# Kernel tuning notes

Hardware: AMD Instinct MI355X
Metric: run time of the kernel (lower is better)

## Reference

```python
import jax, jax.numpy as jnp
import numpy as np

N_NODES = 100000
D_IN = 128
H_DIM = 128
N_EDGES = 1600000


def _gcn_conv(x, src, dst, dinv, W, b):
    # PyG GCNConv(improved=True): h = x @ W; out = A_hat h + b,
    # A_hat = D^{-1/2} (A + 2I) D^{-1/2}
    h = x @ W                                   # [N, H]
    norm = dinv[src] * dinv[dst]                # [E]
    agg = jnp.zeros_like(h).at[dst].add(h[src] * norm[:, None])
    agg = agg + h * (2.0 * dinv * dinv)[:, None]  # self-loop, weight 2.0
    return agg + b


def setup_inputs() -> dict:
    key = jax.random.key(0)
    ks = jax.random.split(key, 12)
    s = 1.0 / np.sqrt(D_IN)
    sh = 1.0 / np.sqrt(2 * H_DIM)
    inp = {
        "x": jax.random.normal(ks[0], (N_NODES, D_IN), jnp.float32),
        "edge_index": jax.random.randint(ks[1], (2, N_EDGES), 0, N_NODES, jnp.int64),
        # GCNConv weights (in -> hidden), bias
        "Wz": jax.random.uniform(ks[2], (D_IN, H_DIM), jnp.float32, -s, s),
        "bz": jnp.zeros((H_DIM,), jnp.float32),
        "Wr": jax.random.uniform(ks[3], (D_IN, H_DIM), jnp.float32, -s, s),
        "br": jnp.zeros((H_DIM,), jnp.float32),
        "Wh": jax.random.uniform(ks[4], (D_IN, H_DIM), jnp.float32, -s, s),
        "bh": jnp.zeros((H_DIM,), jnp.float32),
        # TGCN gate linears: Linear(2h, h)
        "lzW": jax.random.uniform(ks[5], (2 * H_DIM, H_DIM), jnp.float32, -sh, sh),
        "lzb": jax.random.uniform(ks[6], (H_DIM,), jnp.float32, -sh, sh),
        "lrW": jax.random.uniform(ks[7], (2 * H_DIM, H_DIM), jnp.float32, -sh, sh),
        "lrb": jax.random.uniform(ks[8], (H_DIM,), jnp.float32, -sh, sh),
        "lhW": jax.random.uniform(ks[9], (2 * H_DIM, H_DIM), jnp.float32, -sh, sh),
        "lhb": jax.random.uniform(ks[10], (H_DIM,), jnp.float32, -sh, sh),
        # final linear2: hidden -> 1
        "W2": jax.random.uniform(ks[11], (H_DIM, 1), jnp.float32, -1 / np.sqrt(H_DIM), 1 / np.sqrt(H_DIM)),
        "b2": jnp.zeros((1,), jnp.float32),
    }
    return inp


def reference(x, edge_index, Wz, bz, Wr, br, Wh, bh, lzW, lzb, lrW, lrb, lhW, lhb, W2, b2):
    src, dst = edge_index[0], edge_index[1]
    n = x.shape[0]
    # improved GCN norm: deg includes self-loop weight 2
    deg = jnp.zeros((n,), x.dtype).at[dst].add(jnp.ones_like(src, x.dtype)) + 2.0
    dinv = jnp.where(deg > 0, deg ** -0.5, 0.0)
    # TGCN cell with H0 = 0
    H0 = jnp.zeros((n, Wz.shape[1]), x.dtype)
    Z = jax.nn.sigmoid(jnp.concatenate([_gcn_conv(x, src, dst, dinv, Wz, bz), H0], axis=1) @ lzW + lzb)
    R = jax.nn.sigmoid(jnp.concatenate([_gcn_conv(x, src, dst, dinv, Wr, br), H0], axis=1) @ lrW + lrb)
    Ht = jnp.tanh(jnp.concatenate([_gcn_conv(x, src, dst, dinv, Wh, bh), H0 * R], axis=1) @ lhW + lhb)
    H = Z * H0 + (1.0 - Z) * Ht
    # forward: relu output is discarded (y = h overwrites), then linear2
    return H @ W2 + b2
```

## Files before the change

kernel.cpp:

```cpp
#include <hip/hip_runtime.h>
#include <math.h>

#define D 128
#define BSHIFT 9
#define NB 196
#define EPT 7
#define P1B 241
#define CAPB 80
#define PSTRIDE (P1B * CAPB)
#define ECAP 9216
#define P2B NB
#define XCB2 3125
#define PRB 32

typedef __attribute__((ext_vector_type(8))) short s8v;
typedef __attribute__((ext_vector_type(8))) unsigned short us8;
typedef __attribute__((ext_vector_type(4))) unsigned short us4;
typedef __attribute__((ext_vector_type(4))) float f4v;

__device__ __forceinline__ float bf2f(unsigned short u) {
    union { unsigned int i; float f; } v; v.i = ((unsigned int)u) << 16; return v.f;
}
__device__ __forceinline__ unsigned short f2bf(float f) {
    union { float f; unsigned int i; } v; v.f = f;
    unsigned int r = v.i + 0x7FFFu + ((v.i >> 16) & 1u);
    return (unsigned short)(r >> 16);
}

__global__ __launch_bounds__(1024) void k_part1(
    const int* __restrict__ src, const int* __restrict__ dst, int E,
    unsigned int* __restrict__ pairs, int* __restrict__ runlen) {
    __shared__ int cnt[256];
    __shared__ int loff[256];
    __shared__ unsigned int stage[EPT * 1024];
    int bx = blockIdx.x, tid = threadIdx.x;

    unsigned int pk[EPT]; int rkbk[EPT];
    int e0 = bx * (EPT * 1024) + tid;
    if (tid < 256) cnt[tid] = 0;
    __syncthreads();
    #pragma unroll
    for (int i = 0; i < EPT; ++i) {
        int e = e0 + i * 1024;
        bool ok = e < E;
        int d = ok ? dst[e] : 0;
        int s = ok ? src[e] : 0;
        int bk = d >> BSHIFT;
        pk[i] = ((unsigned int)(d & ((1 << BSHIFT) - 1)) << 17) | (unsigned int)s;
        int r = ok ? atomicAdd(&cnt[bk], 1) : 0;
        rkbk[i] = ok ? ((bk << 16) | r) : -1;
    }
    __syncthreads();
    if (tid < 64) {
        int v0 = cnt[tid * 4], v1 = cnt[tid * 4 + 1], v2 = cnt[tid * 4 + 2], v3 = cnt[tid * 4 + 3];
        int s = v0 + v1 + v2 + v3;
        int sc = s;
        #pragma unroll
        for (int off = 1; off < 64; off <<= 1) {
            int o = __shfl_up(sc, off, 64);
            if (tid >= off) sc += o;
        }
        int excl = sc - s;
        loff[tid * 4]     = excl;
        loff[tid * 4 + 1] = excl + v0;
        loff[tid * 4 + 2] = excl + v0 + v1;
        loff[tid * 4 + 3] = excl + v0 + v1 + v2;
    }
    __syncthreads();
    #pragma unroll
    for (int i = 0; i < EPT; ++i) {
        if (rkbk[i] >= 0) {
            int bk = rkbk[i] >> 16;
            stage[loff[bk] + (rkbk[i] & 0xffff)] = pk[i];
        }
    }
    if (tid < 256) runlen[bx * 256 + tid] = cnt[tid];
    __syncthreads();
    int wv = tid >> 6, lane = tid & 63;
    for (int b = wv; b < 256; b += 16) {
        int len = cnt[b];
        if (len == 0) continue;
        int lo = loff[b];
        unsigned int gbase = (unsigned int)b * PSTRIDE + (unsigned int)bx * CAPB;
        for (int j = lane; j < len; j += 64)
            pairs[gbase + j] = stage[lo + j];
    }
}

__global__ __launch_bounds__(1024) void k_mid(
    const unsigned int* __restrict__ pairs, const int* __restrict__ runlen,
    int N,
    int* __restrict__ rowptr, int* __restrict__ deg, float* __restrict__ dinv,
    int* __restrict__ esrc,
    const float* __restrict__ x, unsigned short* __restrict__ xb, int n4,
    const float* __restrict__ Wz, const float* __restrict__ bz,
    const float* __restrict__ lzW, const float* __restrict__ lzb,
    const float* __restrict__ Wh, const float* __restrict__ bh,
    const float* __restrict__ lhW, const float* __restrict__ lhb,
    unsigned short* __restrict__ Mt, float* __restrict__ c) {
    __shared__ int cnt2[512];
    __shared__ int lcur[512];
    __shared__ int rl[256];
    __shared__ int sstage[ECAP];
    __shared__ int stot;
    int bx = blockIdx.x, tid = threadIdx.x;

    if (bx < P2B) {
        int b = bx;
        int n0 = b << BSHIFT;
        int nn = min(N - n0, 1 << BSHIFT);
        long pb = (long)b * PSTRIDE;
        int wv = tid >> 6, lane = tid & 63;

        if (tid < 256) rl[tid] = (tid < P1B) ? runlen[tid * 256 + b] : 0;
        if (tid < 512) cnt2[tid] = 0;
        __syncthreads();
        for (int r = wv; r < P1B; r += 16) {
            int len = rl[r];
            long rb = pb + r * CAPB;
            for (int j = lane; j < len; j += 64)
                atomicAdd(&cnt2[pairs[rb + j] >> 17], 1);
        }
        __syncthreads();
        if (tid < 64) {
            int v[8]; int s = 0;
            #pragma unroll
            for (int k = 0; k < 8; ++k) { v[k] = cnt2[tid * 8 + k]; s += v[k]; }
            int sc = s;
            #pragma unroll
            for (int off = 1; off < 64; off <<= 1) {
                int o = __shfl_up(sc, off, 64);
                if (tid >= off) sc += o;
            }
            int excl = sc - s;
            if (tid == 63) stot = sc;
            #pragma unroll
            for (int k = 0; k < 8; ++k) {
                int node = tid * 8 + k;
                lcur[node] = excl;
                if (node < nn) {
                    rowptr[n0 + node] = b * ECAP + excl;
                    deg[n0 + node]    = v[k];
                    dinv[n0 + node]   = rsqrtf((float)v[k] + 2.0f);
                }
                excl += v[k];
            }
        }
        __syncthreads();
        for (int r = wv; r < P1B; r += 16) {
            int len = rl[r];
            long rb = pb + r * CAPB;
            for (int j = lane; j < len; j += 64) {
                unsigned int p = pairs[rb + j];
                int pos = atomicAdd(&lcur[p >> 17], 1);
                sstage[pos] = (int)(p & 0x1FFFFu);
            }
        }
        __syncthreads();
        int tot = stot;
        for (int i = tid; i < tot; i += 1024)
            esrc[b * ECAP + i] = sstage[i];
    } else if (bx < P2B + XCB2) {
        int i = (bx - P2B) * 1024 + tid;
        if (i < n4) {
            float4 v = ((const float4*)x)[i];
            us4 o;
            o[0] = f2bf(v.x); o[1] = f2bf(v.y); o[2] = f2bf(v.z); o[3] = f2bf(v.w);
            ((us4*)xb)[i] = o;
        }
    } else {
        int k = (bx - (P2B + XCB2)) * 4 + (tid >> 8);
        int j = tid & 255;
        int jj = j & 127;
        const float* W = (j < 128) ? Wz : Wh;
        const float* L = (j < 128) ? lzW : lhW;
        float s = 0.f;
        for (int t = 0; t < 128; ++t) s += W[k * 128 + t] * L[t * 128 + jj];
        Mt[(size_t)j * 128 + k] = f2bf(s);
        if (k == 0) {
            const float* b  = (j < 128) ? bz  : bh;
            const float* lb = (j < 128) ? lzb : lhb;
            float cs = lb[jj];
            for (int t = 0; t < 128; ++t) cs += b[t] * L[t * 128 + jj];
            c[j] = cs;
        }
    }
}

__global__ __launch_bounds__(256) void k_gather(const unsigned short* __restrict__ xb,
                                                const int* __restrict__ esrc,
                                                const int* __restrict__ rowptr,
                                                const int* __restrict__ deg,
                                                const float* __restrict__ dinv,
                                                unsigned short* __restrict__ xab, int N) {
    int node = (blockIdx.x * blockDim.x + threadIdx.x) >> 5;
    int sub  = threadIdx.x & 31;
    if (node >= N) return;
    int eo = sub >> 4, cs = sub & 15;
    int start = rowptr[node];
    int end = start + deg[node];
    float dd = dinv[node];
    us8 xs = {0, 0, 0, 0, 0, 0, 0, 0};
    if (eo == 0) xs = *(const us8*)(xb + (size_t)node * D + cs * 8);
    float acc[8];
    #pragma unroll
    for (int j = 0; j < 8; ++j) acc[j] = 0.f;

    for (int base = start; base < end; base += 32) {
        int cnt = min(32, end - base);
        int myedge = 0; float mynorm = 0.f;
        if (sub < cnt) { myedge = esrc[base + sub]; mynorm = dinv[myedge]; }
        int npairs = (cnt + 1) >> 1;
        int i = 0;
        for (; i + 7 < npairs; i += 8) {
            int i0 = 2 * i + eo;
            int se[8]; float we[8];
            #pragma unroll
            for (int u = 0; u < 8; ++u) {
                se[u] = __shfl(myedge, i0 + 2 * u, 32);
                we[u] = __shfl(mynorm, i0 + 2 * u, 32);
            }
            us8 v[8];
            #pragma unroll
            for (int u = 0; u < 8; ++u)
                v[u] = *(const us8*)(xb + (size_t)se[u] * D + cs * 8);
            #pragma unroll
            for (int u = 0; u < 8; ++u) {
                #pragma unroll
                for (int j = 0; j < 8; ++j) acc[j] += bf2f(v[u][j]) * we[u];
            }
        }
        for (; i + 3 < npairs; i += 4) {
            int i0 = 2 * i + eo;
            int   s0 = __shfl(myedge, i0,     32); float w0 = __shfl(mynorm, i0,     32);
            int   s1 = __shfl(myedge, i0 + 2, 32); float w1 = __shfl(mynorm, i0 + 2, 32);
            int   s2 = __shfl(myedge, i0 + 4, 32); float w2 = __shfl(mynorm, i0 + 4, 32);
            int   s3 = __shfl(myedge, i0 + 6, 32); float w3 = __shfl(mynorm, i0 + 6, 32);
            us8 v0 = *(const us8*)(xb + (size_t)s0 * D + cs * 8);
            us8 v1 = *(const us8*)(xb + (size_t)s1 * D + cs * 8);
            us8 v2 = *(const us8*)(xb + (size_t)s2 * D + cs * 8);
            us8 v3 = *(const us8*)(xb + (size_t)s3 * D + cs * 8);
            #pragma unroll
            for (int j = 0; j < 8; ++j) acc[j] += bf2f(v0[j]) * w0;
            #pragma unroll
            for (int j = 0; j < 8; ++j) acc[j] += bf2f(v1[j]) * w1;
            #pragma unroll
            for (int j = 0; j < 8; ++j) acc[j] += bf2f(v2[j]) * w2;
            #pragma unroll
            for (int j = 0; j < 8; ++j) acc[j] += bf2f(v3[j]) * w3;
        }
        for (; i < npairs; ++i) {
            int i0 = 2 * i + eo;
            int   s0 = __shfl(myedge, i0, 32); float w0 = __shfl(mynorm, i0, 32);
            us8 v0 = *(const us8*)(xb + (size_t)s0 * D + cs * 8);
            #pragma unroll
            for (int j = 0; j < 8; ++j) acc[j] += bf2f(v0[j]) * w0;
        }
    }
    #pragma unroll
    for (int j = 0; j < 8; ++j) acc[j] += __shfl_xor(acc[j], 16);
    if (eo == 0) {
        float sfac = 2.f * dd * dd;
        us8 r;
        #pragma unroll
        for (int j = 0; j < 8; ++j) r[j] = f2bf(acc[j] * dd + bf2f(xs[j]) * sfac);
        *(us8*)(xab + (size_t)node * D + cs * 8) = r;
    }
}

#define ASTRIDE 136
__global__ __launch_bounds__(256, 4) void k_ep_mfma(
    const unsigned short* __restrict__ xab, const unsigned short* __restrict__ Mt,
    const float* __restrict__ c, const float* __restrict__ W2,
    const float* __restrict__ b2, float* __restrict__ out, int N) {
    __shared__ unsigned short Ast[64 * ASTRIDE];
    __shared__ float pbuf[4][64];

    int tid = threadIdx.x;
    int n0 = blockIdx.x * 64;
    int wv = tid >> 6;
    int lane = tid & 63;
    int l = lane & 15, q = lane >> 4;

    #pragma unroll
    for (int j = 0; j < 4; ++j) {
        int idx = tid + 256 * j;
        int row = idx >> 4, c16 = idx & 15;
        us8 v = {0, 0, 0, 0, 0, 0, 0, 0};
        if (n0 + row < N) v = *(const us8*)(xab + (size_t)(n0 + row) * D + c16 * 8);
        *(us8*)&Ast[row * ASTRIDE + c16 * 8] = v;
    }
    __syncthreads();

    int tz0 = 2 * wv;
    f4v acc[4][4];
    #pragma unroll
    for (int i = 0; i < 4; ++i)
        #pragma unroll
        for (int nt = 0; nt < 4; ++nt) acc[i][nt] = (f4v){0.f, 0.f, 0.f, 0.f};

    const unsigned short* Bb = Mt + (size_t)l * 128 + q * 8;

    #pragma unroll
    for (int ks = 0; ks < 4; ++ks) {
        s8v b[4];
        #pragma unroll
        for (int i = 0; i < 2; ++i) {
            b[i]     = *(const s8v*)(Bb + (size_t)(tz0 + i) * 16 * 128 + ks * 32);
            b[2 + i] = *(const s8v*)(Bb + (size_t)(8 + tz0 + i) * 16 * 128 + ks * 32);
        }
        #pragma unroll
        for (int nt = 0; nt < 4; ++nt) {
            s8v a = *(const s8v*)&Ast[(nt * 16 + l) * ASTRIDE + ks * 32 + q * 8];
            #pragma unroll
            for (int i = 0; i < 4; ++i)
                acc[i][nt] = __builtin_amdgcn_mfma_f32_16x16x32_bf16(a, b[i], acc[i][nt], 0, 0, 0);
        }
    }

    float p[4][4];
    #pragma unroll
    for (int nt = 0; nt < 4; ++nt)
        #pragma unroll
        for (int r = 0; r < 4; ++r) p[nt][r] = 0.f;
    #pragma unroll
    for (int i = 0; i < 2; ++i) {
        int col = (tz0 + i) * 16 + l;
        float cz = c[col], ch = c[128 + col], w2 = W2[col];
        #pragma unroll
        for (int nt = 0; nt < 4; ++nt)
            #pragma unroll
            for (int r = 0; r < 4; ++r) {
                float gz = acc[i][nt][r] + cz;
                float gh = acc[2 + i][nt][r] + ch;
                float z  = 1.f / (1.f + __expf(-gz));
                float ht = 1.f - 2.f / (__expf(2.f * gh) + 1.f);
                p[nt][r] += (1.f - z) * ht * w2;
            }
    }
    #pragma unroll
    for (int nt = 0; nt < 4; ++nt)
        #pragma unroll
        for (int r = 0; r < 4; ++r) {
            p[nt][r] += __shfl_xor(p[nt][r], 1);
            p[nt][r] += __shfl_xor(p[nt][r], 2);
            p[nt][r] += __shfl_xor(p[nt][r], 4);
            p[nt][r] += __shfl_xor(p[nt][r], 8);
        }
    if (l == 0) {
        #pragma unroll
        for (int nt = 0; nt < 4; ++nt)
            #pragma unroll
            for (int r = 0; r < 4; ++r)
                pbuf[wv][nt * 16 + q * 4 + r] = p[nt][r];
    }
    __syncthreads();
    if (tid < 64) {
        int n = n0 + tid;
        if (n < N)
            out[n] = pbuf[0][tid] + pbuf[1][tid] + pbuf[2][tid] + pbuf[3][tid] + b2[0];
    }
}

extern "C" void kernel_launch(void* const* d_in, const int* in_sizes, int n_in,
                              void* d_out, int out_size, void* d_ws, size_t ws_size,
                              hipStream_t stream) {
    const float* x    = (const float*)d_in[0];
    const int*   eidx = (const int*)d_in[1];
    const float* Wz   = (const float*)d_in[2];
    const float* bz   = (const float*)d_in[3];
    const float* Wh   = (const float*)d_in[6];
    const float* bh   = (const float*)d_in[7];
    const float* lzW  = (const float*)d_in[8];
    const float* lzb  = (const float*)d_in[9];
    const float* lhW  = (const float*)d_in[12];
    const float* lhb  = (const float*)d_in[13];
    const float* W2   = (const float*)d_in[14];
    const float* b2   = (const float*)d_in[15];
    float* out = (float*)d_out;

    int N = in_sizes[0] / D;
    int E = in_sizes[1] / 2;
    const int* src = eidx;
    const int* dst = eidx + E;

    char* ws = (char*)d_ws;
    size_t off = 0;
    auto alloc = [&](size_t bytes) { void* p = ws + off; off += (bytes + 511) & ~(size_t)511; return p; };
    unsigned short* xb  = (unsigned short*)alloc((size_t)N * D * 2);
    unsigned short* xab = (unsigned short*)alloc((size_t)N * D * 2);
    int*   rowptr = (int*)  alloc((size_t)N * 4);
    int*   deg    = (int*)  alloc((size_t)N * 4);
    float* dinv   = (float*)alloc((size_t)N * 4);
    int*   esrc   = (int*)  alloc((size_t)NB * ECAP * 4);
    int*   runlen = (int*)  alloc((size_t)P1B * 256 * 4);
    unsigned short* Mt = (unsigned short*)alloc(256 * 128 * 2);
    float* c      = (float*)alloc(256 * 4);
    unsigned int* pairs = (unsigned int*)xab;

    int n4 = N * (D / 4);
    k_part1<<<P1B, 1024, 0, stream>>>(src, dst, E, pairs, runlen);
    k_mid<<<P2B + XCB2 + PRB, 1024, 0, stream>>>(
        pairs, runlen, N, rowptr, deg, dinv, esrc,
        x, xb, n4, Wz, bz, lzW, lzb, Wh, bh, lhW, lhb, Mt, c);
    k_gather<<<(N * 32 + 255) / 256, 256, 0, stream>>>(xb, esrc, rowptr, deg, dinv, xab, N);
    k_ep_mfma<<<(N + 63) / 64, 256, 0, stream>>>(xab, Mt, c, W2, b2, out, N);
}
```

Baseline: 238.2 us.

## Fuse neighbor gather into MFMA epilogue and regroup preprocessing kernels

The edge-gather aggregation is merged with the MFMA gate/epilogue kernel, so aggregated rows go straight into shared memory instead of a global bf16 buffer written and then reread. The bucketing pass (part1) now runs in the same launch as the x-to-bf16 conversion and weight folding, and the CSR build (part2) becomes its own kernel. Each node is now gathered by 16 lanes rather than 32, and blocks handle 32 nodes with 512 threads. This drops one intermediate buffer round trip and one launch, but the gather gets less parallelism per node and pairs needs its own workspace allocation.

```diff
diff --git a/kernel.cpp b/kernel.cpp
--- a/kernel.cpp
+++ b/kernel.cpp
@@ -9,7 +9,6 @@
 #define CAPB 80
 #define PSTRIDE (P1B * CAPB)
 #define ECAP 9216
-#define P2B NB
 #define XCB2 3125
 #define PRB 32
 
@@ -27,105 +26,40 @@
     return (unsigned short)(r >> 16);
 }
 
-__global__ __launch_bounds__(1024) void k_part1(
+__global__ __launch_bounds__(1024) void k_pre(
     const int* __restrict__ src, const int* __restrict__ dst, int E,
-    unsigned int* __restrict__ pairs, int* __restrict__ runlen) {
-    __shared__ int cnt[256];
-    __shared__ int loff[256];
-    __shared__ unsigned int stage[EPT * 1024];
-    int bx = blockIdx.x, tid = threadIdx.x;
-
-    unsigned int pk[EPT]; int rkbk[EPT];
-    int e0 = bx * (EPT * 1024) + tid;
-    if (tid < 256) cnt[tid] = 0;
-    __syncthreads();
-    #pragma unroll
-    for (int i = 0; i < EPT; ++i) {
-        int e = e0 + i * 1024;
-        bool ok = e < E;
-        int d = ok ? dst[e] : 0;
-        int s = ok ? src[e] : 0;
-        int bk = d >> BSHIFT;
-        pk[i] = ((unsigned int)(d & ((1 << BSHIFT) - 1)) << 17) | (unsigned int)s;
-        int r = ok ? atomicAdd(&cnt[bk], 1) : 0;
-        rkbk[i] = ok ? ((bk << 16) | r) : -1;
-    }
-    __syncthreads();
-    if (tid < 64) {
-        int v0 = cnt[tid * 4], v1 = cnt[tid * 4 + 1], v2 = cnt[tid * 4 + 2], v3 = cnt[tid * 4 + 3];
-        int s = v0 + v1 + v2 + v3;
-        int sc = s;
-        #pragma unroll
-        for (int off = 1; off < 64; off <<= 1) {
-            int o = __shfl_up(sc, off, 64);
-            if (tid >= off) sc += o;
-        }
-        int excl = sc - s;
-        loff[tid * 4]     = excl;
-        loff[tid * 4 + 1] = excl + v0;
-        loff[tid * 4 + 2] = excl + v0 + v1;
-        loff[tid * 4 + 3] = excl + v0 + v1 + v2;
-    }
-    __syncthreads();
-    #pragma unroll
-    for (int i = 0; i < EPT; ++i) {
-        if (rkbk[i] >= 0) {
-            int bk = rkbk[i] >> 16;
-            stage[loff[bk] + (rkbk[i] & 0xffff)] = pk[i];
-        }
-    }
-    if (tid < 256) runlen[bx * 256 + tid] = cnt[tid];
-    __syncthreads();
-    int wv = tid >> 6, lane = tid & 63;
-    for (int b = wv; b < 256; b += 16) {
-        int len = cnt[b];
-        if (len == 0) continue;
-        int lo = loff[b];
-        unsigned int gbase = (unsigned int)b * PSTRIDE + (unsigned int)bx * CAPB;
-        for (int j = lane; j < len; j += 64)
-            pairs[gbase + j] = stage[lo + j];
-    }
-}
-
-__global__ __launch_bounds__(1024) void k_mid(
-    const unsigned int* __restrict__ pairs, const int* __restrict__ runlen,
-    int N,
-    int* __restrict__ rowptr, int* __restrict__ deg, float* __restrict__ dinv,
-    int* __restrict__ esrc,
+    unsigned int* __restrict__ pairs, int* __restrict__ runlen,
     const float* __restrict__ x, unsigned short* __restrict__ xb, int n4,
     const float* __restrict__ Wz, const float* __restrict__ bz,
     const float* __restrict__ lzW, const float* __restrict__ lzb,
     const float* __restrict__ Wh, const float* __restrict__ bh,
     const float* __restrict__ lhW, const float* __restrict__ lhb,
     unsigned short* __restrict__ Mt, float* __restrict__ c) {
-    __shared__ int cnt2[512];
-    __shared__ int lcur[512];
-    __shared__ int rl[256];
-    __shared__ int sstage[ECAP];
-    __shared__ int stot;
+    __shared__ int cnt[256];
+    __shared__ int loff[256];
+    __shared__ unsigned int stage[EPT * 1024];
     int bx = blockIdx.x, tid = threadIdx.x;
 
-    if (bx < P2B) {
-        int b = bx;
-        int n0 = b << BSHIFT;
-        int nn = min(N - n0, 1 << BSHIFT);
-        long pb = (long)b * PSTRIDE;
-        int wv = tid >> 6, lane = tid & 63;
-
-        if (tid < 256) rl[tid] = (tid < P1B) ? runlen[tid * 256 + b] : 0;
-        if (tid < 512) cnt2[tid] = 0;
+    if (bx < P1B) {
+        unsigned int pk[EPT]; int rkbk[EPT];
+        int e0 = bx * (EPT * 1024) + tid;
+        if (tid < 256) cnt[tid] = 0;
         __syncthreads();
-        for (int r = wv; r < P1B; r += 16) {
-            int len = rl[r];
-            long rb = pb + r * CAPB;
-            for (int j = lane; j < len; j += 64)
-                atomicAdd(&cnt2[pairs[rb + j] >> 17], 1);
+        #pragma unroll
+        for (int i = 0; i < EPT; ++i) {
+            int e = e0 + i * 1024;
+            bool ok = e < E;
+            int d = ok ? dst[e] : 0;
+            int s = ok ? src[e] : 0;
+            int bk = d >> BSHIFT;
+            pk[i] = ((unsigned int)(d & ((1 << BSHIFT) - 1)) << 17) | (unsigned int)s;
+            int r = ok ? atomicAdd(&cnt[bk], 1) : 0;
+            rkbk[i] = ok ? ((bk << 16) | r) : -1;
         }
         __syncthreads();
         if (tid < 64) {
-            int v[8]; int s = 0;
-            #pragma unroll
-            for (int k = 0; k < 8; ++k) { v[k] = cnt2[tid * 8 + k]; s += v[k]; }
+            int v0 = cnt[tid * 4], v1 = cnt[tid * 4 + 1], v2 = cnt[tid * 4 + 2], v3 = cnt[tid * 4 + 3];
+            int s = v0 + v1 + v2 + v3;
             int sc = s;
             #pragma unroll
             for (int off = 1; off < 64; off <<= 1) {
@@ -133,35 +67,32 @@
                 if (tid >= off) sc += o;
             }
             int excl = sc - s;
-            if (tid == 63) stot = sc;
-            #pragma unroll
-            for (int k = 0; k < 8; ++k) {
-                int node = tid * 8 + k;
-                lcur[node] = excl;
-                if (node < nn) {
-                    rowptr[n0 + node] = b * ECAP + excl;
-                    deg[n0 + node]    = v[k];
-                    dinv[n0 + node]   = rsqrtf((float)v[k] + 2.0f);
-                }
-                excl += v[k];
-            }
+            loff[tid * 4]     = excl;
+            loff[tid * 4 + 1] = excl + v0;
+            loff[tid * 4 + 2] = excl + v0 + v1;
+            loff[tid * 4 + 3] = excl + v0 + v1 + v2;
         }
         __syncthreads();
-        for (int r = wv; r < P1B; r += 16) {
-            int len = rl[r];
-            long rb = pb + r * CAPB;
-            for (int j = lane; j < len; j += 64) {
-                unsigned int p = pairs[rb + j];
-                int pos = atomicAdd(&lcur[p >> 17], 1);
-                sstage[pos] = (int)(p & 0x1FFFFu);
-            }
-        }
+        #pragma unroll
+        for (int i = 0; i < EPT; ++i) {
+            if (rkbk[i] >= 0) {
+                int bk = rkbk[i] >> 16;
+                stage[loff[bk] + (rkbk[i] & 0xffff)] = pk[i];
+            }
+        }
+        if (tid < 256) runlen[bx * 256 + tid] = cnt[tid];
         __syncthreads();
-        int tot = stot;
-        for (int i = tid; i < tot; i += 1024)
-            esrc[b * ECAP + i] = sstage[i];
-    } else if (bx < P2B + XCB2) {
-        int i = (bx - P2B) * 1024 + tid;
+        int wv = tid >> 6, lane = tid & 63;
+        for (int b = wv; b < 256; b += 16) {
+            int len = cnt[b];
+            if (len == 0) continue;
+            int lo = loff[b];
+            unsigned int gbase = (unsigned int)b * PSTRIDE + (unsigned int)bx * CAPB;
+            for (int j = lane; j < len; j += 64)
+                pairs[gbase + j] = stage[lo + j];
+        }
+    } else if (bx < P1B + XCB2) {
+        int i = (bx - P1B) * 1024 + tid;
         if (i < n4) {
             float4 v = ((const float4*)x)[i];
             us4 o;
@@ -169,7 +100,7 @@
             ((us4*)xb)[i] = o;
         }
     } else {
-        int k = (bx - (P2B + XCB2)) * 4 + (tid >> 8);
+        int k = (bx - (P1B + XCB2)) * 4 + (tid >> 8);
         int j = tid & 255;
         int jj = j & 127;
         const float* W = (j < 128) ? Wz : Wh;
@@ -187,59 +118,116 @@
     }
 }
 
-__global__ __launch_bounds__(256) void k_gather(const unsigned short* __restrict__ xb,
-                                                const int* __restrict__ esrc,
-                                                const int* __restrict__ rowptr,
-                                                const int* __restrict__ deg,
-                                                const float* __restrict__ dinv,
-                                                unsigned short* __restrict__ xab, int N) {
-    int node = (blockIdx.x * blockDim.x + threadIdx.x) >> 5;
-    int sub  = threadIdx.x & 31;
-    if (node >= N) return;
-    int eo = sub >> 4, cs = sub & 15;
-    int start = rowptr[node];
-    int end = start + deg[node];
-    float dd = dinv[node];
+__global__ __launch_bounds__(1024) void k_part2(
+    const unsigned int* __restrict__ pairs, const int* __restrict__ runlen,
+    int N,
+    int* __restrict__ rowptr, int* __restrict__ deg, float* __restrict__ dinv,
+    int* __restrict__ esrc) {
+    __shared__ int cnt2[512];
+    __shared__ int lcur[512];
+    __shared__ int rl[256];
+    __shared__ int sstage[ECAP];
+    __shared__ int stot;
+    int b = blockIdx.x, tid = threadIdx.x;
+    int n0 = b << BSHIFT;
+    int nn = min(N - n0, 1 << BSHIFT);
+    long pb = (long)b * PSTRIDE;
+    int wv = tid >> 6, lane = tid & 63;
+
+    if (tid < 256) rl[tid] = (tid < P1B) ? runlen[tid * 256 + b] : 0;
+    if (tid < 512) cnt2[tid] = 0;
+    __syncthreads();
+    for (int r = wv; r < P1B; r += 16) {
+        int len = rl[r];
+        long rb = pb + r * CAPB;
+        for (int j = lane; j < len; j += 64)
+            atomicAdd(&cnt2[pairs[rb + j] >> 17], 1);
+    }
+    __syncthreads();
+    if (tid < 64) {
+        int v[8]; int s = 0;
+        #pragma unroll
+        for (int k = 0; k < 8; ++k) { v[k] = cnt2[tid * 8 + k]; s += v[k]; }
+        int sc = s;
+        #pragma unroll
+        for (int off = 1; off < 64; off <<= 1) {
+            int o = __shfl_up(sc, off, 64);
+            if (tid >= off) sc += o;
+        }
+        int excl = sc - s;
+        if (tid == 63) stot = sc;
+        #pragma unroll
+        for (int k = 0; k < 8; ++k) {
+            int node = tid * 8 + k;
+            lcur[node] = excl;
+            if (node < nn) {
+                rowptr[n0 + node] = b * ECAP + excl;
+                deg[n0 + node]    = v[k];
+                dinv[n0 + node]   = rsqrtf((float)v[k] + 2.0f);
+            }
+            excl += v[k];
+        }
+    }
+    __syncthreads();
+    for (int r = wv; r < P1B; r += 16) {
+        int len = rl[r];
+        long rb = pb + r * CAPB;
+        for (int j = lane; j < len; j += 64) {
+            unsigned int p = pairs[rb + j];
+            int pos = atomicAdd(&lcur[p >> 17], 1);
+            sstage[pos] = (int)(p & 0x1FFFFu);
+        }
+    }
+    __syncthreads();
+    int tot = stot;
+    for (int i = tid; i < tot; i += 1024)
+        esrc[b * ECAP + i] = sstage[i];
+}
+
+#define ASTRIDE 136
+__global__ __launch_bounds__(512, 6) void k_gep(
+    const unsigned short* __restrict__ xb,
+    const int* __restrict__ esrc, const int* __restrict__ rowptr,
+    const int* __restrict__ deg, const float* __restrict__ dinv,
+    const unsigned short* __restrict__ Mt, const float* __restrict__ c,
+    const float* __restrict__ W2, const float* __restrict__ b2,
+    float* __restrict__ out, int N) {
+    __shared__ unsigned short Ast[32 * ASTRIDE];
+    __shared__ float pbuf[8][32];
+
+    int tid = threadIdx.x;
+    int n0 = blockIdx.x * 32;
+    int grp = tid >> 4, sub = tid & 15;
+    int node = n0 + grp;
+    bool valid = node < N;
+
+    int start = 0, dcnt = 0;
+    float dd = 0.f;
     us8 xs = {0, 0, 0, 0, 0, 0, 0, 0};
-    if (eo == 0) xs = *(const us8*)(xb + (size_t)node * D + cs * 8);
+    if (valid) {
+        start = rowptr[node];
+        dcnt  = deg[node];
+        dd    = dinv[node];
+        xs = *(const us8*)(xb + (size_t)node * D + sub * 8);
+    }
     float acc[8];
     #pragma unroll
     for (int j = 0; j < 8; ++j) acc[j] = 0.f;
 
-    for (int base = start; base < end; base += 32) {
-        int cnt = min(32, end - base);
+    for (int base = 0; base < dcnt; base += 16) {
+        int cnt = min(16, dcnt - base);
         int myedge = 0; float mynorm = 0.f;
-        if (sub < cnt) { myedge = esrc[base + sub]; mynorm = dinv[myedge]; }
-        int npairs = (cnt + 1) >> 1;
+        if (sub < cnt) { myedge = esrc[start + base + sub]; mynorm = dinv[myedge]; }
         int i = 0;
-        for (; i + 7 < npairs; i += 8) {
-            int i0 = 2 * i + eo;
-            int se[8]; float we[8];
-            #pragma unroll
-            for (int u = 0; u < 8; ++u) {
-                se[u] = __shfl(myedge, i0 + 2 * u, 32);
-                we[u] = __shfl(mynorm, i0 + 2 * u, 32);
-            }
-            us8 v[8];
-            #pragma unroll
-            for (int u = 0; u < 8; ++u)
-                v[u] = *(const us8*)(xb + (size_t)se[u] * D + cs * 8);
-            #pragma unroll
-            for (int u = 0; u < 8; ++u) {
-                #pragma unroll
-                for (int j = 0; j < 8; ++j) acc[j] += bf2f(v[u][j]) * we[u];
-            }
-        }
-        for (; i + 3 < npairs; i += 4) {
-            int i0 = 2 * i + eo;
-            int   s0 = __shfl(myedge, i0,     32); float w0 = __shfl(mynorm, i0,     32);
-            int   s1 = __shfl(myedge, i0 + 2, 32); float w1 = __shfl(mynorm, i0 + 2, 32);
-            int   s2 = __shfl(myedge, i0 + 4, 32); float w2 = __shfl(mynorm, i0 + 4, 32);
-            int   s3 = __shfl(myedge, i0 + 6, 32); float w3 = __shfl(mynorm, i0 + 6, 32);
-            us8 v0 = *(const us8*)(xb + (size_t)s0 * D + cs * 8);
-            us8 v1 = *(const us8*)(xb + (size_t)s1 * D + cs * 8);
-            us8 v2 = *(const us8*)(xb + (size_t)s2 * D + cs * 8);
-            us8 v3 = *(const us8*)(xb + (size_t)s3 * D + cs * 8);
+        for (; i + 3 < cnt; i += 4) {
+            int   s0 = __shfl(myedge, i,     16); float w0 = __shfl(mynorm, i,     16);
+            int   s1 = __shfl(myedge, i + 1, 16); float w1 = __shfl(mynorm, i + 1, 16);
+            int   s2 = __shfl(myedge, i + 2, 16); float w2 = __shfl(mynorm, i + 2, 16);
+            int   s3 = __shfl(myedge, i + 3, 16); float w3 = __shfl(mynorm, i + 3, 16);
+            us8 v0 = *(const us8*)(xb + (size_t)s0 * D + sub * 8);
+            us8 v1 = *(const us8*)(xb + (size_t)s1 * D + sub * 8);
+            us8 v2 = *(const us8*)(xb + (size_t)s2 * D + sub * 8);
+            us8 v3 = *(const us8*)(xb + (size_t)s3 * D + sub * 8);
             #pragma unroll
             for (int j = 0; j < 8; ++j) acc[j] += bf2f(v0[j]) * w0;
             #pragma unroll
@@ -249,116 +237,86 @@
             #pragma unroll
             for (int j = 0; j < 8; ++j) acc[j] += bf2f(v3[j]) * w3;
         }
-        for (; i < npairs; ++i) {
-            int i0 = 2 * i + eo;
-            int   s0 = __shfl(myedge, i0, 32); float w0 = __shfl(mynorm, i0, 32);
-            us8 v0 = *(const us8*)(xb + (size_t)s0 * D + cs * 8);
+        for (; i < cnt; ++i) {
+            int   s0 = __shfl(myedge, i, 16); float w0 = __shfl(mynorm, i, 16);
+            us8 v0 = *(const us8*)(xb + (size_t)s0 * D + sub * 8);
             #pragma unroll
             for (int j = 0; j < 8; ++j) acc[j] += bf2f(v0[j]) * w0;
         }
     }
-    #pragma unroll
-    for (int j = 0; j < 8; ++j) acc[j] += __shfl_xor(acc[j], 16);
-    if (eo == 0) {
+    {
         float sfac = 2.f * dd * dd;
         us8 r;
         #pragma unroll
         for (int j = 0; j < 8; ++j) r[j] = f2bf(acc[j] * dd + bf2f(xs[j]) * sfac);
-        *(us8*)(xab + (size_t)node * D + cs * 8) = r;
-    }
-}
-
-#define ASTRIDE 136
-__global__ __launch_bounds__(256, 4) void k_ep_mfma(
-    const unsigned short* __restrict__ xab, const unsigned short* __restrict__ Mt,
-    const float* __restrict__ c, const float* __restrict__ W2,
-    const float* __restrict__ b2, float* __restrict__ out, int N) {
-    __shared__ unsigned short Ast[64 * ASTRIDE];
-    __shared__ float pbuf[4][64];
-
-    int tid = threadIdx.x;
-    int n0 = blockIdx.x * 64;
+        *(us8*)&Ast[grp * ASTRIDE + sub * 8] = r;
+    }
+    __syncthreads();
+
     int wv = tid >> 6;
     int lane = tid & 63;
     int l = lane & 15, q = lane >> 4;
 
+    f4v acc2[2][2];
     #pragma unroll
-    for (int j = 0; j < 4; ++j) {
-        int idx = tid + 256 * j;
-        int row = idx >> 4, c16 = idx & 15;
-        us8 v = {0, 0, 0, 0, 0, 0, 0, 0};
-        if (n0 + row < N) v = *(const us8*)(xab + (size_t)(n0 + row) * D + c16 * 8);
-        *(us8*)&Ast[row * ASTRIDE + c16 * 8] = v;
-    }
-    __syncthreads();
-
-    int tz0 = 2 * wv;
-    f4v acc[4][4];
-    #pragma unroll
-    for (int i = 0; i < 4; ++i)
-        #pragma unroll
-        for (int nt = 0; nt < 4; ++nt) acc[i][nt] = (f4v){0.f, 0.f, 0.f, 0.f};
+    for (int zi = 0; zi < 2; ++zi)
+        #pragma unroll
+        for (int nt = 0; nt < 2; ++nt) acc2[zi][nt] = (f4v){0.f, 0.f, 0.f, 0.f};
 
     const unsigned short* Bb = Mt + (size_t)l * 128 + q * 8;
 
     #pragma unroll
     for (int ks = 0; ks < 4; ++ks) {
-        s8v b[4];
-        #pragma unroll
-        for (int i = 0; i < 2; ++i) {
-            b[i]     = *(const s8v*)(Bb + (size_t)(tz0 + i) * 16 * 128 + ks * 32);
-            b[2 + i] = *(const s8v*)(Bb + (size_t)(8 + tz0 + i) * 16 * 128 + ks * 32);
-        }
-        #pragma unroll
-        for (int nt = 0; nt < 4; ++nt) {
+        s8v bz_ = *(const s8v*)(Bb + (size_t)wv * 16 * 128 + ks * 32);
+        s8v bh_ = *(const s8v*)(Bb + (size_t)(8 + wv) * 16 * 128 + ks * 32);
+        #pragma unroll
+        for (int nt = 0; nt < 2; ++nt) {
             s8v a = *(const s8v*)&Ast[(nt * 16 + l) * ASTRIDE + ks * 32 + q * 8];
-            #pragma unroll
-            for (int i = 0; i < 4; ++i)
-                acc[i][nt] = __builtin_amdgcn_mfma_f32_16x16x32_bf16(a, b[i], acc[i][nt], 0, 0, 0);
-        }
-    }
-
-    float p[4][4];
-    #pragma unroll
-    for (int nt = 0; nt < 4; ++nt)
-        #pragma unroll
-        for (int r = 0; r < 4; ++r) p[nt][r] = 0.f;
-    #pragma unroll
-    for (int i = 0; i < 2; ++i) {
-        int col = (tz0 + i) * 16 + l;
+            acc2[0][nt] = __builtin_amdgcn_mfma_f32_16x16x32_bf16(a, bz_, acc2[0][nt], 0, 0, 0);
+            acc2[1][nt] = __builtin_amdgcn_mfma_f32_16x16x32_bf16(a, bh_, acc2[1][nt], 0, 0, 0);
+        }
+    }
+
+    {
+        int col = wv * 16 + l;
         float cz = c[col], ch = c[128 + col], w2 = W2[col];
-        #pragma unroll
-        for (int nt = 0; nt < 4; ++nt)
+        float p[2][4];
+        #pragma unroll
+        for (int nt = 0; nt < 2; ++nt)
             #pragma unroll
             for (int r = 0; r < 4; ++r) {
-                float gz = acc[i][nt][r] + cz;
-                float gh = acc[2 + i][nt][r] + ch;
+                float gz = acc2[0][nt][r] + cz;
+                float gh = acc2[1][nt][r] + ch;
                 float z  = 1.f / (1.f + __expf(-gz));
                 float ht = 1.f - 2.f / (__expf(2.f * gh) + 1.f);
-                p[nt][r] += (1.f - z) * ht * w2;
-            }
-    }
-    #pragma unroll
-    for (int nt = 0; nt < 4; ++nt)
-        #pragma unroll
-        for (int r = 0; r < 4; ++r) {
-            p[nt][r] += __shfl_xor(p[nt][r], 1);
-            p[nt][r] += __shfl_xor(p[nt][r], 2);
-            p[nt][r] += __shfl_xor(p[nt][r], 4);
-            p[nt][r] += __shfl_xor(p[nt][r], 8);
-        }
-    if (l == 0) {
-        #pragma unroll
-        for (int nt = 0; nt < 4; ++nt)
-            #pragma unroll
-            for (int r = 0; r < 4; ++r)
-                pbuf[wv][nt * 16 + q * 4 + r] = p[nt][r];
-    }
-    __syncthreads();
-    if (tid < 64) {
+                p[nt][r] = (1.f - z) * ht * w2;
+            }
+        #pragma unroll
+        for (int nt = 0; nt < 2; ++nt)
+            #pragma unroll
+            for (int r = 0; r < 4; ++r) {
+                p[nt][r] += __shfl_xor(p[nt][r], 1);
+                p[nt][r] += __shfl_xor(p[nt][r], 2);
+                p[nt][r] += __shfl_xor(p[nt][r], 4);
+                p[nt][r] += __shfl_xor(p[nt][r], 8);
+            }
+        if (l == 0) {
+            #pragma unroll
+            for (int nt = 0; nt < 2; ++nt)
+                #pragma unroll
+                for (int r = 0; r < 4; ++r)
+                    pbuf[wv][nt * 16 + q * 4 + r] = p[nt][r];
+        }
+    }
+    __syncthreads();
+    if (tid < 32) {
         int n = n0 + tid;
-        if (n < N)
-            out[n] = pbuf[0][tid] + pbuf[1][tid] + pbuf[2][tid] + pbuf[3][tid] + b2[0];
+        if (n < N) {
+            float s = b2[0];
+            #pragma unroll
+            for (int cp = 0; cp < 8; ++cp) s += pbuf[cp][tid];
+            out[n] = s;
+        }
     }
 }
 
@@ -388,7 +346,7 @@
     size_t off = 0;
     auto alloc = [&](size_t bytes) { void* p = ws + off; off += (bytes + 511) & ~(size_t)511; return p; };
     unsigned short* xb  = (unsigned short*)alloc((size_t)N * D * 2);
-    unsigned short* xab = (unsigned short*)alloc((size_t)N * D * 2);
+    unsigned int*   pairs = (unsigned int*)alloc((size_t)NB * PSTRIDE * 4);
     int*   rowptr = (int*)  alloc((size_t)N * 4);
     int*   deg    = (int*)  alloc((size_t)N * 4);
     float* dinv   = (float*)alloc((size_t)N * 4);
@@ -396,13 +354,12 @@
     int*   runlen = (int*)  alloc((size_t)P1B * 256 * 4);
     unsigned short* Mt = (unsigned short*)alloc(256 * 128 * 2);
     float* c      = (float*)alloc(256 * 4);
-    unsigned int* pairs = (unsigned int*)xab;
 
     int n4 = N * (D / 4);
-    k_part1<<<P1B, 1024, 0, stream>>>(src, dst, E, pairs, runlen);
-    k_mid<<<P2B + XCB2 + PRB, 1024, 0, stream>>>(
-        pairs, runlen, N, rowptr, deg, dinv, esrc,
+    k_pre<<<P1B + XCB2 + PRB, 1024, 0, stream>>>(
+        src, dst, E, pairs, runlen,
         x, xb, n4, Wz, bz, lzW, lzb, Wh, bh, lhW, lhb, Mt, c);
-    k_gather<<<(N * 32 + 255) / 256, 256, 0, stream>>>(xb, esrc, rowptr, deg, dinv, xab, N);
-    k_ep_mfma<<<(N + 63) / 64, 256, 0, stream>>>(xab, Mt, c, W2, b2, out, N);
-}
+    k_part2<<<NB, 1024, 0, stream>>>(pairs, runlen, N, rowptr, deg, dinv, esrc);
+    k_gep<<<(N + 31) / 32, 512, 0, stream>>>(
+        xb, esrc, rowptr, deg, dinv, Mt, c, W2, b2, out, N);
+}
```

Measured after the change: 231.2 us. 2.9% less time.

## Fuse x conversion and weight precompute into partition pass, split second pass out

Applied to the files above, without the earlier changes.

Moves the x-to-bf16 conversion and the fused weight-product precompute from the second partition kernel into the first one, so they run alongside the edge bucketing instead of the bucket compaction. The second partition step becomes its own small kernel. Each conversion block now handles four float4 chunks per thread, which cuts the block count. The gather kernel drops its 8-wide unrolled edge loop and loads the self feature only after accumulation, trading memory-level parallelism for lower register pressure.

```diff
diff --git a/kernel.cpp b/kernel.cpp
--- a/kernel.cpp
+++ b/kernel.cpp
@@ -9,8 +9,7 @@
 #define CAPB 80
 #define PSTRIDE (P1B * CAPB)
 #define ECAP 9216
-#define P2B NB
-#define XCB2 3125
+#define XCB4 782
 #define PRB 32
 
 typedef __attribute__((ext_vector_type(8))) short s8v;
@@ -27,105 +26,40 @@
     return (unsigned short)(r >> 16);
 }
 
-__global__ __launch_bounds__(1024) void k_part1(
+__global__ __launch_bounds__(1024) void k_pre(
     const int* __restrict__ src, const int* __restrict__ dst, int E,
-    unsigned int* __restrict__ pairs, int* __restrict__ runlen) {
-    __shared__ int cnt[256];
-    __shared__ int loff[256];
-    __shared__ unsigned int stage[EPT * 1024];
-    int bx = blockIdx.x, tid = threadIdx.x;
-
-    unsigned int pk[EPT]; int rkbk[EPT];
-    int e0 = bx * (EPT * 1024) + tid;
-    if (tid < 256) cnt[tid] = 0;
-    __syncthreads();
-    #pragma unroll
-    for (int i = 0; i < EPT; ++i) {
-        int e = e0 + i * 1024;
-        bool ok = e < E;
-        int d = ok ? dst[e] : 0;
-        int s = ok ? src[e] : 0;
-        int bk = d >> BSHIFT;
-        pk[i] = ((unsigned int)(d & ((1 << BSHIFT) - 1)) << 17) | (unsigned int)s;
-        int r = ok ? atomicAdd(&cnt[bk], 1) : 0;
-        rkbk[i] = ok ? ((bk << 16) | r) : -1;
-    }
-    __syncthreads();
-    if (tid < 64) {
-        int v0 = cnt[tid * 4], v1 = cnt[tid * 4 + 1], v2 = cnt[tid * 4 + 2], v3 = cnt[tid * 4 + 3];
-        int s = v0 + v1 + v2 + v3;
-        int sc = s;
-        #pragma unroll
-        for (int off = 1; off < 64; off <<= 1) {
-            int o = __shfl_up(sc, off, 64);
-            if (tid >= off) sc += o;
-        }
-        int excl = sc - s;
-        loff[tid * 4]     = excl;
-        loff[tid * 4 + 1] = excl + v0;
-        loff[tid * 4 + 2] = excl + v0 + v1;
-        loff[tid * 4 + 3] = excl + v0 + v1 + v2;
-    }
-    __syncthreads();
-    #pragma unroll
-    for (int i = 0; i < EPT; ++i) {
-        if (rkbk[i] >= 0) {
-            int bk = rkbk[i] >> 16;
-            stage[loff[bk] + (rkbk[i] & 0xffff)] = pk[i];
-        }
-    }
-    if (tid < 256) runlen[bx * 256 + tid] = cnt[tid];
-    __syncthreads();
-    int wv = tid >> 6, lane = tid & 63;
-    for (int b = wv; b < 256; b += 16) {
-        int len = cnt[b];
-        if (len == 0) continue;
-        int lo = loff[b];
-        unsigned int gbase = (unsigned int)b * PSTRIDE + (unsigned int)bx * CAPB;
-        for (int j = lane; j < len; j += 64)
-            pairs[gbase + j] = stage[lo + j];
-    }
-}
-
-__global__ __launch_bounds__(1024) void k_mid(
-    const unsigned int* __restrict__ pairs, const int* __restrict__ runlen,
-    int N,
-    int* __restrict__ rowptr, int* __restrict__ deg, float* __restrict__ dinv,
-    int* __restrict__ esrc,
+    unsigned int* __restrict__ pairs, int* __restrict__ runlen,
     const float* __restrict__ x, unsigned short* __restrict__ xb, int n4,
     const float* __restrict__ Wz, const float* __restrict__ bz,
     const float* __restrict__ lzW, const float* __restrict__ lzb,
     const float* __restrict__ Wh, const float* __restrict__ bh,
     const float* __restrict__ lhW, const float* __restrict__ lhb,
     unsigned short* __restrict__ Mt, float* __restrict__ c) {
-    __shared__ int cnt2[512];
-    __shared__ int lcur[512];
-    __shared__ int rl[256];
-    __shared__ int sstage[ECAP];
-    __shared__ int stot;
+    __shared__ int cnt[256];
+    __shared__ int loff[256];
+    __shared__ unsigned int stage[EPT * 1024];
     int bx = blockIdx.x, tid = threadIdx.x;
 
-    if (bx < P2B) {
-        int b = bx;
-        int n0 = b << BSHIFT;
-        int nn = min(N - n0, 1 << BSHIFT);
-        long pb = (long)b * PSTRIDE;
-        int wv = tid >> 6, lane = tid & 63;
-
-        if (tid < 256) rl[tid] = (tid < P1B) ? runlen[tid * 256 + b] : 0;
-        if (tid < 512) cnt2[tid] = 0;
+    if (bx < P1B) {
+        unsigned int pk[EPT]; int rkbk[EPT];
+        int e0 = bx * (EPT * 1024) + tid;
+        if (tid < 256) cnt[tid] = 0;
         __syncthreads();
-        for (int r = wv; r < P1B; r += 16) {
-            int len = rl[r];
-            long rb = pb + r * CAPB;
-            for (int j = lane; j < len; j += 64)
-                atomicAdd(&cnt2[pairs[rb + j] >> 17], 1);
+        #pragma unroll
+        for (int i = 0; i < EPT; ++i) {
+            int e = e0 + i * 1024;
+            bool ok = e < E;
+            int d = ok ? dst[e] : 0;
+            int s = ok ? src[e] : 0;
+            int bk = d >> BSHIFT;
+            pk[i] = ((unsigned int)(d & ((1 << BSHIFT) - 1)) << 17) | (unsigned int)s;
+            int r = ok ? atomicAdd(&cnt[bk], 1) : 0;
+            rkbk[i] = ok ? ((bk << 16) | r) : -1;
         }
         __syncthreads();
         if (tid < 64) {
-            int v[8]; int s = 0;
-            #pragma unroll
-            for (int k = 0; k < 8; ++k) { v[k] = cnt2[tid * 8 + k]; s += v[k]; }
+            int v0 = cnt[tid * 4], v1 = cnt[tid * 4 + 1], v2 = cnt[tid * 4 + 2], v3 = cnt[tid * 4 + 3];
+            int s = v0 + v1 + v2 + v3;
             int sc = s;
             #pragma unroll
             for (int off = 1; off < 64; off <<= 1) {
@@ -133,43 +67,44 @@
                 if (tid >= off) sc += o;
             }
             int excl = sc - s;
-            if (tid == 63) stot = sc;
-            #pragma unroll
-            for (int k = 0; k < 8; ++k) {
-                int node = tid * 8 + k;
-                lcur[node] = excl;
-                if (node < nn) {
-                    rowptr[n0 + node] = b * ECAP + excl;
-                    deg[n0 + node]    = v[k];
-                    dinv[n0 + node]   = rsqrtf((float)v[k] + 2.0f);
-                }
-                excl += v[k];
-            }
+            loff[tid * 4]     = excl;
+            loff[tid * 4 + 1] = excl + v0;
+            loff[tid * 4 + 2] = excl + v0 + v1;
+            loff[tid * 4 + 3] = excl + v0 + v1 + v2;
         }
         __syncthreads();
-        for (int r = wv; r < P1B; r += 16) {
-            int len = rl[r];
-            long rb = pb + r * CAPB;
-            for (int j = lane; j < len; j += 64) {
-                unsigned int p = pairs[rb + j];
-                int pos = atomicAdd(&lcur[p >> 17], 1);
-                sstage[pos] = (int)(p & 0x1FFFFu);
-            }
-        }
+        #pragma unroll
+        for (int i = 0; i < EPT; ++i) {
+            if (rkbk[i] >= 0) {
+                int bk = rkbk[i] >> 16;
+                stage[loff[bk] + (rkbk[i] & 0xffff)] = pk[i];
+            }
+        }
+        if (tid < 256) runlen[bx * 256 + tid] = cnt[tid];
         __syncthreads();
-        int tot = stot;
-        for (int i = tid; i < tot; i += 1024)
-            esrc[b * ECAP + i] = sstage[i];
-    } else if (bx < P2B + XCB2) {
-        int i = (bx - P2B) * 1024 + tid;
-        if (i < n4) {
-            float4 v = ((const float4*)x)[i];
-            us4 o;
-            o[0] = f2bf(v.x); o[1] = f2bf(v.y); o[2] = f2bf(v.z); o[3] = f2bf(v.w);
-            ((us4*)xb)[i] = o;
+        int wv = tid >> 6, lane = tid & 63;
+        for (int b = wv; b < 256; b += 16) {
+            int len = cnt[b];
+            if (len == 0) continue;
+            int lo = loff[b];
+            unsigned int gbase = (unsigned int)b * PSTRIDE + (unsigned int)bx * CAPB;
+            for (int j = lane; j < len; j += 64)
+                pairs[gbase + j] = stage[lo + j];
+        }
+    } else if (bx < P1B + XCB4) {
+        int i0 = (bx - P1B) * 4096 + tid;
+        #pragma unroll
+        for (int u = 0; u < 4; ++u) {
+            int i = i0 + u * 1024;
+            if (i < n4) {
+                float4 v = ((const float4*)x)[i];
+                us4 o;
+                o[0] = f2bf(v.x); o[1] = f2bf(v.y); o[2] = f2bf(v.z); o[3] = f2bf(v.w);
+                ((us4*)xb)[i] = o;
+            }
         }
     } else {
-        int k = (bx - (P2B + XCB2)) * 4 + (tid >> 8);
+        int k = (bx - (P1B + XCB4)) * 4 + (tid >> 8);
         int j = tid & 255;
         int jj = j & 127;
         const float* W = (j < 128) ? Wz : Wh;
@@ -187,6 +122,72 @@
     }
 }
 
+__global__ __launch_bounds__(1024) void k_part2(
+    const unsigned int* __restrict__ pairs, const int* __restrict__ runlen,
+    int N,
+    int* __restrict__ rowptr, int* __restrict__ deg, float* __restrict__ dinv,
+    int* __restrict__ esrc) {
+    __shared__ int cnt2[512];
+    __shared__ int lcur[512];
+    __shared__ int rl[256];
+    __shared__ int sstage[ECAP];
+    __shared__ int stot;
+    int b = blockIdx.x, tid = threadIdx.x;
+    int n0 = b << BSHIFT;
+    int nn = min(N - n0, 1 << BSHIFT);
+    long pb = (long)b * PSTRIDE;
+    int wv = tid >> 6, lane = tid & 63;
+
+    if (tid < 256) rl[tid] = (tid < P1B) ? runlen[tid * 256 + b] : 0;
+    if (tid < 512) cnt2[tid] = 0;
+    __syncthreads();
+    for (int r = wv; r < P1B; r += 16) {
+        int len = rl[r];
+        long rb = pb + r * CAPB;
+        for (int j = lane; j < len; j += 64)
+            atomicAdd(&cnt2[pairs[rb + j] >> 17], 1);
+    }
+    __syncthreads();
+    if (tid < 64) {
+        int v[8]; int s = 0;
+        #pragma unroll
+        for (int k = 0; k < 8; ++k) { v[k] = cnt2[tid * 8 + k]; s += v[k]; }
+        int sc = s;
+        #pragma unroll
+        for (int off = 1; off < 64; off <<= 1) {
+            int o = __shfl_up(sc, off, 64);
+            if (tid >= off) sc += o;
+        }
+        int excl = sc - s;
+        if (tid == 63) stot = sc;
+        #pragma unroll
+        for (int k = 0; k < 8; ++k) {
+            int node = tid * 8 + k;
+            lcur[node] = excl;
+            if (node < nn) {
+                rowptr[n0 + node] = b * ECAP + excl;
+                deg[n0 + node]    = v[k];
+                dinv[n0 + node]   = rsqrtf((float)v[k] + 2.0f);
+            }
+            excl += v[k];
+        }
+    }
+    __syncthreads();
+    for (int r = wv; r < P1B; r += 16) {
+        int len = rl[r];
+        long rb = pb + r * CAPB;
+        for (int j = lane; j < len; j += 64) {
+            unsigned int p = pairs[rb + j];
+            int pos = atomicAdd(&lcur[p >> 17], 1);
+            sstage[pos] = (int)(p & 0x1FFFFu);
+        }
+    }
+    __syncthreads();
+    int tot = stot;
+    for (int i = tid; i < tot; i += 1024)
+        esrc[b * ECAP + i] = sstage[i];
+}
+
 __global__ __launch_bounds__(256) void k_gather(const unsigned short* __restrict__ xb,
                                                 const int* __restrict__ esrc,
                                                 const int* __restrict__ rowptr,
@@ -200,8 +201,6 @@
     int start = rowptr[node];
     int end = start + deg[node];
     float dd = dinv[node];
-    us8 xs = {0, 0, 0, 0, 0, 0, 0, 0};
-    if (eo == 0) xs = *(const us8*)(xb + (size_t)node * D + cs * 8);
     float acc[8];
     #pragma unroll
     for (int j = 0; j < 8; ++j) acc[j] = 0.f;
@@ -210,27 +209,9 @@
         int cnt = min(32, end - base);
         int myedge = 0; float mynorm = 0.f;
         if (sub < cnt) { myedge = esrc[base + sub]; mynorm = dinv[myedge]; }
-        int npairs = (cnt + 1) >> 1;
+        int pairs = (cnt + 1) >> 1;
         int i = 0;
-        for (; i + 7 < npairs; i += 8) {
-            int i0 = 2 * i + eo;
-            int se[8]; float we[8];
-            #pragma unroll
-            for (int u = 0; u < 8; ++u) {
-                se[u] = __shfl(myedge, i0 + 2 * u, 32);
-                we[u] = __shfl(mynorm, i0 + 2 * u, 32);
-            }
-            us8 v[8];
-            #pragma unroll
-            for (int u = 0; u < 8; ++u)
-                v[u] = *(const us8*)(xb + (size_t)se[u] * D + cs * 8);
-            #pragma unroll
-            for (int u = 0; u < 8; ++u) {
-                #pragma unroll
-                for (int j = 0; j < 8; ++j) acc[j] += bf2f(v[u][j]) * we[u];
-            }
-        }
-        for (; i + 3 < npairs; i += 4) {
+        for (; i + 3 < pairs; i += 4) {
             int i0 = 2 * i + eo;
             int   s0 = __shfl(myedge, i0,     32); float w0 = __shfl(mynorm, i0,     32);
             int   s1 = __shfl(myedge, i0 + 2, 32); float w1 = __shfl(mynorm, i0 + 2, 32);
@@ -249,7 +230,7 @@
             #pragma unroll
             for (int j = 0; j < 8; ++j) acc[j] += bf2f(v3[j]) * w3;
         }
-        for (; i < npairs; ++i) {
+        for (; i < pairs; ++i) {
             int i0 = 2 * i + eo;
             int   s0 = __shfl(myedge, i0, 32); float w0 = __shfl(mynorm, i0, 32);
             us8 v0 = *(const us8*)(xb + (size_t)s0 * D + cs * 8);
@@ -260,6 +241,7 @@
     #pragma unroll
     for (int j = 0; j < 8; ++j) acc[j] += __shfl_xor(acc[j], 16);
     if (eo == 0) {
+        us8 xs = *(const us8*)(xb + (size_t)node * D + cs * 8);
         float sfac = 2.f * dd * dd;
         us8 r;
         #pragma unroll
@@ -399,10 +381,10 @@
     unsigned int* pairs = (unsigned int*)xab;
 
     int n4 = N * (D / 4);
-    k_part1<<<P1B, 1024, 0, stream>>>(src, dst, E, pairs, runlen);
-    k_mid<<<P2B + XCB2 + PRB, 1024, 0, stream>>>(
-        pairs, runlen, N, rowptr, deg, dinv, esrc,
+    k_pre<<<P1B + XCB4 + PRB, 1024, 0, stream>>>(
+        src, dst, E, pairs, runlen,
         x, xb, n4, Wz, bz, lzW, lzb, Wh, bh, lhW, lhb, Mt, c);
+    k_part2<<<NB, 1024, 0, stream>>>(pairs, runlen, N, rowptr, deg, dinv, esrc);
     k_gather<<<(N * 32 + 255) / 256, 256, 0, stream>>>(xb, esrc, rowptr, deg, dinv, xab, N);
     k_ep_mfma<<<(N + 63) / 64, 256, 0, stream>>>(xab, Mt, c, W2, b2, out, N);
 }
```

Result: faster. 231.4 us (-2.8%).
